# Performance work log

Measured on AMD Instinct MI355X. Metric: run time of the kernel, lower is better.

The kernel has to match this reference:

```python
import jax, jax.numpy as jnp
import numpy as np

L, H, N = 8192, 1024, 1024
MAX_PHASE = 6.283


def setup_inputs() -> dict:
    key = jax.random.key(0)
    ks = jax.random.split(key, 9)
    input_real = jax.random.uniform(ks[0], (L, H), dtype=jnp.float32)
    input_imag = jax.random.uniform(ks[1], (L, H), dtype=jnp.float32)
    # LRU parameter init (r_min=0, r_max=1, max_phase=6.283)
    u1 = jax.random.uniform(ks[2], (N,), dtype=jnp.float32)
    u2 = jax.random.uniform(ks[3], (N,), dtype=jnp.float32)
    nu_log = jnp.log(-0.5 * jnp.log(u1))
    theta_log = jnp.log(u2 * MAX_PHASE)
    B_real = jax.random.normal(ks[4], (N, H), dtype=jnp.float32) / np.float32(np.sqrt(2 * H))
    B_imag = jax.random.normal(ks[5], (N, H), dtype=jnp.float32) / np.float32(np.sqrt(2 * H))
    C_real = jax.random.normal(ks[6], (H, N), dtype=jnp.float32) / np.float32(np.sqrt(N))
    C_imag = jax.random.normal(ks[7], (H, N), dtype=jnp.float32) / np.float32(np.sqrt(N))
    D = jax.random.normal(ks[8], (H,), dtype=jnp.float32)
    diag_lambda = jnp.exp(jax.lax.complex(-jnp.exp(nu_log), jnp.exp(theta_log)))
    gamma_log = jnp.log(jnp.sqrt(1.0 - jnp.abs(diag_lambda) ** 2))
    return dict(input_real=input_real, input_imag=input_imag,
                nu_log=nu_log, theta_log=theta_log,
                B_real=B_real, B_imag=B_imag,
                C_real=C_real, C_imag=C_imag,
                D=D, gamma_log=gamma_log)


def _binop(e_i, e_j):
    a_i, bu_i = e_i
    a_j, bu_j = e_j
    return a_j * a_i, a_j * bu_i + bu_j


def _lru_forward(input_real, input_imag, nu_log, theta_log,
                 B_real, B_imag, C_real, C_imag, D, gamma_log):
    u = jax.lax.complex(input_real, input_imag)                      # (L, H) complex
    Lambda = jnp.exp(jax.lax.complex(-jnp.exp(nu_log), jnp.exp(theta_log)))  # (N,)
    # Faithful to source: exp(i * gamma_log), NOT exp(gamma_log)
    exp_gamma = jnp.exp(jax.lax.complex(jnp.zeros_like(gamma_log), gamma_log))  # (N,)
    B_norm = jax.lax.complex(B_real, B_imag) * exp_gamma[:, None]    # (N, H)
    Bu = jnp.einsum('lh,nh->ln', u, B_norm)                          # (L, N)
    Lambda_el = jnp.broadcast_to(Lambda[None, :], Bu.shape)          # (L, N)
    _, x = jax.lax.associative_scan(_binop, (Lambda_el, Bu))         # (L, N) states
    C = jax.lax.complex(C_real, C_imag)                              # (H, N)
    Dc = D.astype(C.dtype)                                           # (H,) complex
    y = jnp.real(jnp.einsum('ln,hn->lh', x, C)) + jnp.real(Dc[None, :] * u)
    return y                                                         # (L, H) float32


def reference(input_real, input_imag, nu_log, theta_log,
              B_real, B_imag, C_real, C_imag, D, gamma_log):
    return _lru_forward(input_real, input_imag, nu_log, theta_log,
                        B_real, B_imag, C_real, C_imag, D, gamma_log)
```

## Files before the change

kernel.cpp:

```cpp
#include <hip/hip_runtime.h>
#include <math.h>

#define L_SEQ 8192
#define H_DIM 1024
#define N_DIM 1024
#define K2    2048
#define NCHUNK 64
#define CHUNK 128

typedef unsigned short u16;
typedef __attribute__((ext_vector_type(8))) __bf16 bf16x8;
typedef __attribute__((ext_vector_type(4))) float  f32x4;

__device__ __forceinline__ u16 f2bf(float x) {
    unsigned int u = __float_as_uint(x);
    u = (u + 0x7fffu + ((u >> 16) & 1u)) >> 16;
    return (u16)u;
}
__device__ __forceinline__ float bf2f(u16 h) {
    return __uint_as_float(((unsigned int)h) << 16);
}

__device__ __forceinline__ void gload_lds16(const void* g, void* s) {
    __builtin_amdgcn_global_load_lds(
        (const __attribute__((address_space(1))) unsigned int*)g,
        (__attribute__((address_space(3))) unsigned int*)s, 16, 0, 0);
}

__global__ void lru_lambda(const float* __restrict__ nu_log,
                           const float* __restrict__ theta_log,
                           float* __restrict__ Lr, float* __restrict__ Li) {
    int n = blockIdx.x * 256 + threadIdx.x;
    float nu  = expf(nu_log[n]);
    float th  = expf(theta_log[n]);
    float mag = expf(-nu);
    Lr[n] = mag * cosf(th);
    Li[n] = mag * sinf(th);
}

__global__ void pack_u(const float* __restrict__ R, const float* __restrict__ I,
                       u16* __restrict__ A) {
    size_t t = (size_t)blockIdx.x * 256 + threadIdx.x;
    size_t base = t * 4;
    int lrow = (int)(base >> 10);
    int h    = (int)(base & 1023);
    float4 r  = *reinterpret_cast<const float4*>(R + base);
    float4 im = *reinterpret_cast<const float4*>(I + base);
    u16* p0 = A + ((size_t)lrow << 11) + h;
    *reinterpret_cast<ushort4*>(p0) =
        make_ushort4(f2bf(r.x), f2bf(r.y), f2bf(r.z), f2bf(r.w));
    *reinterpret_cast<ushort4*>(p0 + 1024) =
        make_ushort4(f2bf(im.x), f2bf(im.y), f2bf(im.z), f2bf(im.w));
}

__global__ void bnorm_pack(const float* __restrict__ Br, const float* __restrict__ Bi,
                           const float* __restrict__ G, u16* __restrict__ Bp) {
    size_t t = (size_t)blockIdx.x * 256 + threadIdx.x;
    size_t base = t * 4;
    int n = (int)(base >> 10);
    int h = (int)(base & 1023);
    float g = G[n];
    float sg, cg;
    sincosf(g, &sg, &cg);
    float4 br = *reinterpret_cast<const float4*>(Br + base);
    float4 bi = *reinterpret_cast<const float4*>(Bi + base);
    float nr0 = br.x * cg - bi.x * sg, ni0 = br.x * sg + bi.x * cg;
    float nr1 = br.y * cg - bi.y * sg, ni1 = br.y * sg + bi.y * cg;
    float nr2 = br.z * cg - bi.z * sg, ni2 = br.z * sg + bi.z * cg;
    float nr3 = br.w * cg - bi.w * sg, ni3 = br.w * sg + bi.w * cg;
    u16* row0 = Bp + (size_t)n * K2;
    u16* row1 = Bp + (size_t)(N_DIM + n) * K2;
    *reinterpret_cast<ushort4*>(row0 + h) =
        make_ushort4(f2bf(nr0), f2bf(nr1), f2bf(nr2), f2bf(nr3));
    *reinterpret_cast<ushort4*>(row0 + 1024 + h) =
        make_ushort4(f2bf(-ni0), f2bf(-ni1), f2bf(-ni2), f2bf(-ni3));
    *reinterpret_cast<ushort4*>(row1 + h) =
        make_ushort4(f2bf(ni0), f2bf(ni1), f2bf(ni2), f2bf(ni3));
    *reinterpret_cast<ushort4*>(row1 + 1024 + h) =
        make_ushort4(f2bf(nr0), f2bf(nr1), f2bf(nr2), f2bf(nr3));
}

__global__ void pack_C(const float* __restrict__ Cr, const float* __restrict__ Ci,
                       u16* __restrict__ Cp) {
    size_t t = (size_t)blockIdx.x * 256 + threadIdx.x;
    size_t base = t * 4;
    int h = (int)(base >> 10);
    int n = (int)(base & 1023);
    float4 cr = *reinterpret_cast<const float4*>(Cr + base);
    float4 ci = *reinterpret_cast<const float4*>(Ci + base);
    u16* row = Cp + (size_t)h * K2;
    *reinterpret_cast<ushort4*>(row + n) =
        make_ushort4(f2bf(cr.x), f2bf(cr.y), f2bf(cr.z), f2bf(cr.w));
    *reinterpret_cast<ushort4*>(row + 1024 + n) =
        make_ushort4(f2bf(-ci.x), f2bf(-ci.y), f2bf(-ci.z), f2bf(-ci.w));
}

template <int EPI, int WMF>
__global__ __launch_bounds__(512, 2) void gemm_pipe(
    const u16* __restrict__ A, const u16* __restrict__ B, int Klen, int lda,
    u16* __restrict__ OutB, float* __restrict__ OutF, int ldo,
    const float* __restrict__ Dv, const float* __restrict__ Ur) {
    constexpr int BM     = WMF * 32;
    constexpr int BN     = 256;
    constexpr int ABYTES = BM * 128;
    constexpr int SLOT   = (BM + BN) * 128;
    __shared__ __attribute__((aligned(128))) char lds[2 * SLOT];
    const int tid = threadIdx.x;
    const int l   = tid & 63;
    const int w   = tid >> 6;
    const int wm  = w >> 2;
    const int wn  = w & 3;
    const long bm = (long)blockIdx.x * BM;
    const long bn = (long)blockIdx.y * BN;

    f32x4 acc[WMF][4];
#pragma unroll
    for (int i = 0; i < WMF; ++i)
#pragma unroll
        for (int j = 0; j < 4; ++j) acc[i][j] = (f32x4){0.f, 0.f, 0.f, 0.f};

    const int    swzcol    = (((tid & 7) ^ ((tid >> 3) & 7)) << 4);
    const size_t rowstride = (size_t)lda * 2;
    const size_t a_src0    = (size_t)(bm + (tid >> 3)) * rowstride + swzcol;
    const size_t b_src0    = (size_t)(bn + (tid >> 3)) * rowstride + swzcol;
    const char*  Agb       = (const char*)A;
    const char*  Bgb       = (const char*)B;

    auto STAGE = [&](int kt, int sl) {
        const size_t kofs = (size_t)kt * 128;
        char* la = lds + sl * SLOT + tid * 16;
        char* lb = lds + sl * SLOT + ABYTES + tid * 16;
#pragma unroll
        for (int j = 0; j < BM / 64; ++j)
            gload_lds16(Agb + a_src0 + (size_t)j * 64 * rowstride + kofs,
                        la + j * 8192);
#pragma unroll
        for (int j = 0; j < 4; ++j)
            gload_lds16(Bgb + b_src0 + (size_t)j * 64 * rowstride + kofs,
                        lb + j * 8192);
    };

    const int l15   = l & 15;
    const int lslot = l >> 4;

    const int nt = Klen / 64;
    STAGE(0, 0);
    STAGE(1, 1);

    for (int t = 0; t < nt; ++t) {
        const int s = t & 1;
        if (t < nt - 1) {
            if constexpr (BM == 256) asm volatile("s_waitcnt vmcnt(8)" ::: "memory");
            else                     asm volatile("s_waitcnt vmcnt(6)" ::: "memory");
        } else {
            asm volatile("s_waitcnt vmcnt(0)" ::: "memory");
        }
        __builtin_amdgcn_sched_barrier(0);
        __builtin_amdgcn_s_barrier();
        __builtin_amdgcn_sched_barrier(0);

        const char* lA = lds + s * SLOT;
        const char* lB = lA + ABYTES;
#pragma unroll
        for (int kk = 0; kk < 2; ++kk) {
            bf16x8 af[WMF], bg[4];
#pragma unroll
            for (int mi = 0; mi < WMF; ++mi) {
                int r   = wm * (WMF * 16) + mi * 16 + l15;
                int sl3 = ((kk << 2) | lslot) ^ (r & 7);
                af[mi]  = *reinterpret_cast<const bf16x8*>(lA + r * 128 + sl3 * 16);
            }
#pragma unroll
            for (int ni = 0; ni < 4; ++ni) {
                int r   = wn * 64 + ni * 16 + l15;
                int sl3 = ((kk << 2) | lslot) ^ (r & 7);
                bg[ni]  = *reinterpret_cast<const bf16x8*>(lB + r * 128 + sl3 * 16);
            }
            __builtin_amdgcn_s_setprio(1);
#pragma unroll
            for (int mi = 0; mi < WMF; ++mi)
#pragma unroll
                for (int ni = 0; ni < 4; ++ni)
                    acc[mi][ni] = __builtin_amdgcn_mfma_f32_16x16x32_bf16(
                        af[mi], bg[ni], acc[mi][ni], 0, 0, 0);
            __builtin_amdgcn_s_setprio(0);
        }
        __builtin_amdgcn_sched_barrier(0);
        __builtin_amdgcn_s_barrier();
        __builtin_amdgcn_sched_barrier(0);
        if (t + 2 < nt) STAGE(t + 2, s);
    }

#pragma unroll
    for (int mi = 0; mi < WMF; ++mi) {
        const long row0 = bm + wm * (WMF * 16) + mi * 16 + ((l >> 4) << 2);
#pragma unroll
        for (int ni = 0; ni < 4; ++ni) {
            const long col = bn + wn * 64 + ni * 16 + l15;
            if (EPI == 0) {
#pragma unroll
                for (int r = 0; r < 4; ++r)
                    OutB[(size_t)(row0 + r) * ldo + col] = f2bf(acc[mi][ni][r]);
            } else {
                const float d = Dv[col];
#pragma unroll
                for (int r = 0; r < 4; ++r) {
                    size_t o = (size_t)(row0 + r) * ldo + col;
                    OutF[o] = acc[mi][ni][r] + d * Ur[o];
                }
            }
        }
    }
}

__global__ void scan_local(u16* __restrict__ X,
                           const float* __restrict__ Lr, const float* __restrict__ Li,
                           float* __restrict__ Acr, float* __restrict__ Aci,
                           float* __restrict__ bcr, float* __restrict__ bci) {
    int n = blockIdx.y * 256 + threadIdx.x;
    int c = blockIdx.x;
    float lr = Lr[n], li = Li[n];
    float sr = 0.f, si = 0.f, pr = 1.f, pi = 0.f;
    size_t base = (size_t)c * CHUNK * K2 + n;
    for (int j = 0; j < CHUNK; ++j) {
        size_t idx = base + (size_t)j * K2;
        float br = bf2f(X[idx]), bi = bf2f(X[idx + 1024]);
        float nr = lr * sr - li * si + br;
        float ni = lr * si + li * sr + bi;
        sr = nr; si = ni;
        X[idx] = f2bf(sr); X[idx + 1024] = f2bf(si);
        float qr = lr * pr - li * pi;
        float qi = lr * pi + li * pr;
        pr = qr; pi = qi;
    }
    Acr[c * N_DIM + n] = pr; Aci[c * N_DIM + n] = pi;
    bcr[c * N_DIM + n] = sr; bci[c * N_DIM + n] = si;
}

__global__ void scan_carry(const float* __restrict__ Acr, const float* __restrict__ Aci,
                           const float* __restrict__ bcr, const float* __restrict__ bci,
                           float* __restrict__ car, float* __restrict__ cai) {
    int n = blockIdx.x * 256 + threadIdx.x;
    float sr = 0.f, si = 0.f;
    for (int c = 0; c < NCHUNK; ++c) {
        car[c * N_DIM + n] = sr; cai[c * N_DIM + n] = si;
        float ar = Acr[c * N_DIM + n], ai = Aci[c * N_DIM + n];
        float nr = ar * sr - ai * si + bcr[c * N_DIM + n];
        float ni = ar * si + ai * sr + bci[c * N_DIM + n];
        sr = nr; si = ni;
    }
}

__global__ void scan_fix(u16* __restrict__ X,
                         const float* __restrict__ Lr, const float* __restrict__ Li,
                         const float* __restrict__ car, const float* __restrict__ cai) {
    int n = blockIdx.y * 256 + threadIdx.x;
    int c = blockIdx.x + 1;
    float lr = Lr[n], li = Li[n];
    float cr = car[c * N_DIM + n], ci = cai[c * N_DIM + n];
    float pr = lr * cr - li * ci;
    float pi = lr * ci + li * cr;
    size_t base = (size_t)c * CHUNK * K2 + n;
    for (int j = 0; j < CHUNK; ++j) {
        size_t idx = base + (size_t)j * K2;
        X[idx]        = f2bf(bf2f(X[idx]) + pr);
        X[idx + 1024] = f2bf(bf2f(X[idx + 1024]) + pi);
        float qr = lr * pr - li * pi;
        float qi = lr * pi + li * pr;
        pr = qr; pi = qi;
    }
}

extern "C" void kernel_launch(void* const* d_in, const int* in_sizes, int n_in,
                              void* d_out, int out_size, void* d_ws, size_t ws_size,
                              hipStream_t stream) {
    (void)in_sizes; (void)n_in; (void)out_size; (void)ws_size;
    const float* input_real = (const float*)d_in[0];
    const float* input_imag = (const float*)d_in[1];
    const float* nu_log     = (const float*)d_in[2];
    const float* theta_log  = (const float*)d_in[3];
    const float* B_real     = (const float*)d_in[4];
    const float* B_imag     = (const float*)d_in[5];
    const float* C_real     = (const float*)d_in[6];
    const float* C_imag     = (const float*)d_in[7];
    const float* D          = (const float*)d_in[8];
    const float* gamma_log  = (const float*)d_in[9];
    float* y = (float*)d_out;

    char* ws = (char*)d_ws;
    float* Lr  = (float*)(ws);
    float* Li  = (float*)(ws + (4 << 10));
    float* Acr = (float*)(ws + (8 << 10));
    float* Aci = Acr + NCHUNK * N_DIM;
    float* bcr = Aci + NCHUNK * N_DIM;
    float* bci = bcr + NCHUNK * N_DIM;
    float* car = bci + NCHUNK * N_DIM;
    float* cai = car + NCHUNK * N_DIM;
    u16* Ap   = (u16*)(ws + ((size_t)2 << 20));
    u16* Cp   = Ap;
    u16* Bp   = (u16*)(ws + ((size_t)34 << 20));
    u16* X    = (u16*)(ws + ((size_t)42 << 20));

    lru_lambda<<<N_DIM / 256, 256, 0, stream>>>(nu_log, theta_log, Lr, Li);
    pack_u<<<(L_SEQ * H_DIM / 4) / 256, 256, 0, stream>>>(input_real, input_imag, Ap);
    bnorm_pack<<<(N_DIM * H_DIM / 4) / 256, 256, 0, stream>>>(B_real, B_imag, gamma_log, Bp);
    gemm_pipe<0, 8><<<dim3(L_SEQ / 256, K2 / 256), 512, 0, stream>>>(
        Ap, Bp, K2, K2, X, nullptr, K2, nullptr, nullptr);
    scan_local<<<dim3(NCHUNK, N_DIM / 256), 256, 0, stream>>>(X, Lr, Li, Acr, Aci, bcr, bci);
    scan_carry<<<N_DIM / 256, 256, 0, stream>>>(Acr, Aci, bcr, bci, car, cai);
    scan_fix<<<dim3(NCHUNK - 1, N_DIM / 256), 256, 0, stream>>>(X, Lr, Li, car, cai);
    pack_C<<<(H_DIM * N_DIM / 4) / 256, 256, 0, stream>>>(C_real, C_imag, Cp);
    gemm_pipe<1, 4><<<dim3(L_SEQ / 128, H_DIM / 256), 512, 0, stream>>>(
        X, Cp, K2, K2, nullptr, y, H_DIM, D, input_real);
}
```

Baseline: 183.6 us.

## Software-pipeline LDS fragment loads with MFMA in GEMM main loop

Restructures the K-loop so the LDS reads for the next half-tile (kk=1, then the next stage's kk=0) are issued before the MFMAs of the current half-tile. The intent is to hide LDS read latency behind matrix instructions, at the cost of double-buffered fragment registers. The global-to-LDS prefetch waits and barriers are reordered to match. The extra registers can lower occupancy, and the reordered waits and barriers risk subtle races.

```diff
diff --git a/kernel.cpp b/kernel.cpp
--- a/kernel.cpp
+++ b/kernel.cpp
@@ -143,52 +143,76 @@
     const int l15   = l & 15;
     const int lslot = l >> 4;
 
+    auto LOADA = [&](bf16x8 (&af)[WMF], const char* lA, int kk) {
+#pragma unroll
+        for (int mi = 0; mi < WMF; ++mi) {
+            int r   = wm * (WMF * 16) + mi * 16 + l15;
+            int sl3 = ((kk << 2) | lslot) ^ (r & 7);
+            af[mi]  = *reinterpret_cast<const bf16x8*>(lA + r * 128 + sl3 * 16);
+        }
+    };
+    auto LOADB = [&](bf16x8 (&bg)[4], const char* lB, int kk) {
+#pragma unroll
+        for (int ni = 0; ni < 4; ++ni) {
+            int r   = wn * 64 + ni * 16 + l15;
+            int sl3 = ((kk << 2) | lslot) ^ (r & 7);
+            bg[ni]  = *reinterpret_cast<const bf16x8*>(lB + r * 128 + sl3 * 16);
+        }
+    };
+    auto MM = [&](bf16x8 (&af)[WMF], bf16x8 (&bg)[4], int nlo) {
+        __builtin_amdgcn_s_setprio(1);
+#pragma unroll
+        for (int mi = 0; mi < WMF; ++mi)
+#pragma unroll
+            for (int nj = 0; nj < 2; ++nj)
+                acc[mi][nlo + nj] = __builtin_amdgcn_mfma_f32_16x16x32_bf16(
+                    af[mi], bg[nlo + nj], acc[mi][nlo + nj], 0, 0, 0);
+        __builtin_amdgcn_s_setprio(0);
+    };
+
     const int nt = Klen / 64;
     STAGE(0, 0);
     STAGE(1, 1);
+    if constexpr (BM == 256) asm volatile("s_waitcnt vmcnt(8)" ::: "memory");
+    else                     asm volatile("s_waitcnt vmcnt(6)" ::: "memory");
+    __builtin_amdgcn_sched_barrier(0);
+    __builtin_amdgcn_s_barrier();
+    __builtin_amdgcn_sched_barrier(0);
+
+    bf16x8 afX[WMF], afY[WMF], bgX[4], bgY[4];
+    LOADA(afX, lds, 0);
+    LOADB(bgX, lds + ABYTES, 0);
 
     for (int t = 0; t < nt; ++t) {
         const int s = t & 1;
-        if (t < nt - 1) {
-            if constexpr (BM == 256) asm volatile("s_waitcnt vmcnt(8)" ::: "memory");
-            else                     asm volatile("s_waitcnt vmcnt(6)" ::: "memory");
-        } else {
-            asm volatile("s_waitcnt vmcnt(0)" ::: "memory");
-        }
+        const char* lA = lds + s * SLOT;
+        const char* lB = lA + ABYTES;
+        LOADA(afY, lA, 1);
+        LOADB(bgY, lB, 1);
+        MM(afX, bgX, 0);
+        MM(afX, bgX, 2);
+        asm volatile("s_waitcnt lgkmcnt(0)" ::: "memory");
         __builtin_amdgcn_sched_barrier(0);
         __builtin_amdgcn_s_barrier();
         __builtin_amdgcn_sched_barrier(0);
-
-        const char* lA = lds + s * SLOT;
-        const char* lB = lA + ABYTES;
-#pragma unroll
-        for (int kk = 0; kk < 2; ++kk) {
-            bf16x8 af[WMF], bg[4];
-#pragma unroll
-            for (int mi = 0; mi < WMF; ++mi) {
-                int r   = wm * (WMF * 16) + mi * 16 + l15;
-                int sl3 = ((kk << 2) | lslot) ^ (r & 7);
-                af[mi]  = *reinterpret_cast<const bf16x8*>(lA + r * 128 + sl3 * 16);
-            }
-#pragma unroll
-            for (int ni = 0; ni < 4; ++ni) {
-                int r   = wn * 64 + ni * 16 + l15;
-                int sl3 = ((kk << 2) | lslot) ^ (r & 7);
-                bg[ni]  = *reinterpret_cast<const bf16x8*>(lB + r * 128 + sl3 * 16);
-            }
-            __builtin_amdgcn_s_setprio(1);
-#pragma unroll
-            for (int mi = 0; mi < WMF; ++mi)
-#pragma unroll
-                for (int ni = 0; ni < 4; ++ni)
-                    acc[mi][ni] = __builtin_amdgcn_mfma_f32_16x16x32_bf16(
-                        af[mi], bg[ni], acc[mi][ni], 0, 0, 0);
-            __builtin_amdgcn_s_setprio(0);
-        }
-        __builtin_amdgcn_sched_barrier(0);
-        __builtin_amdgcn_s_barrier();
-        __builtin_amdgcn_sched_barrier(0);
-        if (t + 2 < nt) STAGE(t + 2, s);
+        if (t + 2 < nt) {
+            STAGE(t + 2, s);
+            if constexpr (BM == 256) asm volatile("s_waitcnt vmcnt(8)" ::: "memory");
+            else                     asm volatile("s_waitcnt vmcnt(6)" ::: "memory");
+        } else if (t + 1 < nt) {
+            asm volatile("s_waitcnt vmcnt(0)" ::: "memory");
+        }
+        if (t + 1 < nt) {
+            __builtin_amdgcn_sched_barrier(0);
+            __builtin_amdgcn_s_barrier();
+            __builtin_amdgcn_sched_barrier(0);
+            const char* lA2 = lds + (s ^ 1) * SLOT;
+            const char* lB2 = lA2 + ABYTES;
+            LOADA(afX, lA2, 0);
+            LOADB(bgX, lB2, 0);
+        }
+        MM(afY, bgY, 0);
+        MM(afY, bgY, 2);
     }
 
 #pragma unroll
```

Result: no change. 182.4 us (-0.6%).

## Restructure GEMM main loop into 8-phase quadrant pipeline with split staging

Applied to the files above, without the earlier changes.

Replaces the simple double-buffered K loop in both GEMMs with an 8-phase schedule. Each phase loads a half-tile of A or B into LDS, reads register fragments for the next quadrant, and issues MFMAs on one quadrant of the output tile. The aim is to interleave global-to-LDS loads, LDS reads and MFMA work more finely so memory latency hides behind compute. In exchange it adds a barrier and an lgkmcnt wait per phase, and it uses more registers for the ping-pong fragment sets.

```diff
diff --git a/kernel.cpp b/kernel.cpp
--- a/kernel.cpp
+++ b/kernel.cpp
@@ -96,22 +96,24 @@
 }
 
 template <int EPI, int WMF>
-__global__ __launch_bounds__(512, 2) void gemm_pipe(
+__global__ __launch_bounds__(512, 2) void gemm8p(
     const u16* __restrict__ A, const u16* __restrict__ B, int Klen, int lda,
     u16* __restrict__ OutB, float* __restrict__ OutF, int ldo,
     const float* __restrict__ Dv, const float* __restrict__ Ur) {
-    constexpr int BM     = WMF * 32;
-    constexpr int BN     = 256;
-    constexpr int ABYTES = BM * 128;
-    constexpr int SLOT   = (BM + BN) * 128;
-    __shared__ __attribute__((aligned(128))) char lds[2 * SLOT];
+    constexpr int BM    = WMF * 32;
+    constexpr int AMF   = WMF / 2;
+    constexpr int GA    = BM / 128;
+    constexpr int AH    = (BM / 2) * 128;
+    constexpr int BH    = 16384;
+    constexpr int DBUFB = 2 * AH + 2 * BH;
+    __shared__ __attribute__((aligned(128))) char lds[2 * DBUFB];
     const int tid = threadIdx.x;
     const int l   = tid & 63;
     const int w   = tid >> 6;
     const int wm  = w >> 2;
     const int wn  = w & 3;
     const long bm = (long)blockIdx.x * BM;
-    const long bn = (long)blockIdx.y * BN;
+    const long bn = (long)blockIdx.y * 256;
 
     f32x4 acc[WMF][4];
 #pragma unroll
@@ -119,77 +121,154 @@
 #pragma unroll
         for (int j = 0; j < 4; ++j) acc[i][j] = (f32x4){0.f, 0.f, 0.f, 0.f};
 
-    const int    swzcol    = (((tid & 7) ^ ((tid >> 3) & 7)) << 4);
+    const int lr  = tid >> 3;
+    const int lrh = lr >> 5, lrl = lr & 31;
+    const int swzcol = ((tid & 7) ^ (lr & 7)) << 4;
     const size_t rowstride = (size_t)lda * 2;
-    const size_t a_src0    = (size_t)(bm + (tid >> 3)) * rowstride + swzcol;
-    const size_t b_src0    = (size_t)(bn + (tid >> 3)) * rowstride + swzcol;
-    const char*  Agb       = (const char*)A;
-    const char*  Bgb       = (const char*)B;
-
-    auto STAGE = [&](int kt, int sl) {
-        const size_t kofs = (size_t)kt * 128;
-        char* la = lds + sl * SLOT + tid * 16;
-        char* lb = lds + sl * SLOT + ABYTES + tid * 16;
-#pragma unroll
-        for (int j = 0; j < BM / 64; ++j)
-            gload_lds16(Agb + a_src0 + (size_t)j * 64 * rowstride + kofs,
-                        la + j * 8192);
-#pragma unroll
-        for (int j = 0; j < 4; ++j)
-            gload_lds16(Bgb + b_src0 + (size_t)j * 64 * rowstride + kofs,
-                        lb + j * 8192);
-    };
+    const char* Agb = (const char*)A;
+    const char* Bgb = (const char*)B;
+    size_t a_src[2][GA];
+#pragma unroll
+    for (int h = 0; h < 2; ++h)
+#pragma unroll
+        for (int j = 0; j < GA; ++j) {
+            int row = (BM == 256) ? (j * 128 + h * 64 + lr)
+                                  : (lrh * 64 + h * 32 + lrl);
+            a_src[h][j] = (size_t)(bm + row) * rowstride + swzcol;
+        }
+    size_t b_src[2][2];
+#pragma unroll
+    for (int h = 0; h < 2; ++h)
+#pragma unroll
+        for (int j = 0; j < 2; ++j) {
+            int row = j * 128 + lrh * 64 + h * 32 + lrl;
+            b_src[h][j] = (size_t)(bn + row) * rowstride + swzcol;
+        }
 
     const int l15   = l & 15;
     const int lslot = l >> 4;
-
-    const int nt = Klen / 64;
-    STAGE(0, 0);
-    STAGE(1, 1);
-
-    for (int t = 0; t < nt; ++t) {
-        const int s = t & 1;
-        if (t < nt - 1) {
-            if constexpr (BM == 256) asm volatile("s_waitcnt vmcnt(8)" ::: "memory");
-            else                     asm volatile("s_waitcnt vmcnt(6)" ::: "memory");
-        } else {
-            asm volatile("s_waitcnt vmcnt(0)" ::: "memory");
-        }
-        __builtin_amdgcn_sched_barrier(0);
-        __builtin_amdgcn_s_barrier();
-        __builtin_amdgcn_sched_barrier(0);
-
-        const char* lA = lds + s * SLOT;
-        const char* lB = lA + ABYTES;
+    int aoff[AMF][2], boff[2][2];
+#pragma unroll
+    for (int mi = 0; mi < AMF; ++mi)
 #pragma unroll
         for (int kk = 0; kk < 2; ++kk) {
-            bf16x8 af[WMF], bg[4];
-#pragma unroll
-            for (int mi = 0; mi < WMF; ++mi) {
-                int r   = wm * (WMF * 16) + mi * 16 + l15;
-                int sl3 = ((kk << 2) | lslot) ^ (r & 7);
-                af[mi]  = *reinterpret_cast<const bf16x8*>(lA + r * 128 + sl3 * 16);
-            }
-#pragma unroll
-            for (int ni = 0; ni < 4; ++ni) {
-                int r   = wn * 64 + ni * 16 + l15;
-                int sl3 = ((kk << 2) | lslot) ^ (r & 7);
-                bg[ni]  = *reinterpret_cast<const bf16x8*>(lB + r * 128 + sl3 * 16);
-            }
-            __builtin_amdgcn_s_setprio(1);
-#pragma unroll
-            for (int mi = 0; mi < WMF; ++mi)
-#pragma unroll
-                for (int ni = 0; ni < 4; ++ni)
-                    acc[mi][ni] = __builtin_amdgcn_mfma_f32_16x16x32_bf16(
-                        af[mi], bg[ni], acc[mi][ni], 0, 0, 0);
-            __builtin_amdgcn_s_setprio(0);
-        }
-        __builtin_amdgcn_sched_barrier(0);
-        __builtin_amdgcn_s_barrier();
-        __builtin_amdgcn_sched_barrier(0);
-        if (t + 2 < nt) STAGE(t + 2, s);
-    }
+            int rr = wm * (BM / 4) + mi * 16 + l15;
+            aoff[mi][kk] = rr * 128 + ((((kk << 2) | lslot) ^ (rr & 7)) << 4);
+        }
+#pragma unroll
+    for (int ni = 0; ni < 2; ++ni)
+#pragma unroll
+        for (int kk = 0; kk < 2; ++kk) {
+            int rr = wn * 32 + ni * 16 + l15;
+            boff[ni][kk] = rr * 128 + ((((kk << 2) | lslot) ^ (rr & 7)) << 4);
+        }
+
+    const int nt    = Klen / 64;
+    const int niter = nt / 2;
+
+    bf16x8 aE[2 * AMF], aO[2 * AMF], bE[4], bO[4];
+
+#define STAGE_A(KT, H) do { if ((KT) < nt) {                                 \
+    char* _d = lds + ((KT) & 1) * DBUFB + (H) * AH + tid * 16;               \
+    _Pragma("unroll") for (int j = 0; j < GA; ++j)                           \
+        gload_lds16(Agb + a_src[H][j] + (size_t)(KT) * 128, _d + j * 8192);  \
+    } } while (0)
+#define STAGE_B(KT, H) do { if ((KT) < nt) {                                 \
+    char* _d = lds + ((KT) & 1) * DBUFB + 2 * AH + (H) * BH + tid * 16;      \
+    _Pragma("unroll") for (int j = 0; j < 2; ++j)                            \
+        gload_lds16(Bgb + b_src[H][j] + (size_t)(KT) * 128, _d + j * 8192);  \
+    } } while (0)
+#define READ_A(DST, QM, DB) {                                                \
+    _Pragma("unroll") for (int mi = 0; mi < AMF; ++mi)                       \
+        _Pragma("unroll") for (int kk = 0; kk < 2; ++kk)                     \
+            DST[mi * 2 + kk] = *reinterpret_cast<const bf16x8*>(             \
+                lds + (DB) * DBUFB + (QM) * AH + aoff[mi][kk]); }
+#define READ_B(DST, QN, DB) {                                                \
+    _Pragma("unroll") for (int ni = 0; ni < 2; ++ni)                         \
+        _Pragma("unroll") for (int kk = 0; kk < 2; ++kk)                     \
+            DST[ni * 2 + kk] = *reinterpret_cast<const bf16x8*>(             \
+                lds + (DB) * DBUFB + 2 * AH + (QN) * BH + boff[ni][kk]); }
+#define MFMA_Q(ASET, BSET, QM, QN) {                                         \
+    __builtin_amdgcn_s_setprio(1);                                           \
+    _Pragma("unroll") for (int mi = 0; mi < AMF; ++mi)                       \
+        _Pragma("unroll") for (int ni = 0; ni < 2; ++ni)                     \
+            _Pragma("unroll") for (int kk = 0; kk < 2; ++kk)                 \
+                acc[(QM) * AMF + mi][(QN) * 2 + ni] =                        \
+                    __builtin_amdgcn_mfma_f32_16x16x32_bf16(                 \
+                        ASET[mi * 2 + kk], BSET[ni * 2 + kk],                \
+                        acc[(QM) * AMF + mi][(QN) * 2 + ni], 0, 0, 0);       \
+    __builtin_amdgcn_s_setprio(0); }
+#define VMW do { if constexpr (WMF == 8)                                     \
+        asm volatile("s_waitcnt vmcnt(6)" ::: "memory");                     \
+    else asm volatile("s_waitcnt vmcnt(4)" ::: "memory"); } while (0)
+#define BAR1 do { __builtin_amdgcn_sched_barrier(0);                         \
+    __builtin_amdgcn_s_barrier();                                            \
+    __builtin_amdgcn_sched_barrier(0); } while (0)
+#define ENDPH do { asm volatile("s_waitcnt lgkmcnt(0)" ::: "memory");        \
+    __builtin_amdgcn_sched_barrier(0);                                       \
+    __builtin_amdgcn_s_barrier();                                            \
+    __builtin_amdgcn_sched_barrier(0); } while (0)
+
+    STAGE_B(0, 0); STAGE_A(0, 0); STAGE_A(0, 1); STAGE_B(0, 1);
+    STAGE_B(1, 0); STAGE_A(1, 0); STAGE_A(1, 1);
+    VMW;
+    BAR1;
+    READ_A(aE, 0, 0); READ_B(bE, 0, 0);
+    asm volatile("s_waitcnt lgkmcnt(0)" ::: "memory");
+
+    for (int i = 0; i < niter; ++i) {
+        const int t2 = 2 * i;
+        STAGE_B(t2 + 1, 1);
+        BAR1;
+        READ_A(aO, 1, 0);
+        MFMA_Q(aE, bE, 0, 0);
+        ENDPH;
+        STAGE_B(t2 + 2, 0);
+        BAR1;
+        READ_B(bO, 1, 0);
+        MFMA_Q(aO, bE, 1, 0);
+        ENDPH;
+        STAGE_A(t2 + 2, 0);
+        BAR1;
+        MFMA_Q(aE, bO, 0, 1);
+        ENDPH;
+        STAGE_A(t2 + 2, 1);
+        if (i + 1 < niter) { VMW; }
+        else { asm volatile("s_waitcnt vmcnt(0)" ::: "memory"); }
+        BAR1;
+        READ_A(aE, 0, 1); READ_B(bE, 0, 1);
+        MFMA_Q(aO, bO, 1, 1);
+        ENDPH;
+        STAGE_B(t2 + 2, 1);
+        BAR1;
+        READ_A(aO, 1, 1);
+        MFMA_Q(aE, bE, 0, 0);
+        ENDPH;
+        STAGE_B(t2 + 3, 0);
+        BAR1;
+        READ_B(bO, 1, 1);
+        MFMA_Q(aO, bE, 1, 0);
+        ENDPH;
+        STAGE_A(t2 + 3, 0);
+        BAR1;
+        MFMA_Q(aE, bO, 0, 1);
+        ENDPH;
+        STAGE_A(t2 + 3, 1);
+        VMW;
+        BAR1;
+        if (i + 1 < niter) { READ_A(aE, 0, 0); READ_B(bE, 0, 0); }
+        MFMA_Q(aO, bO, 1, 1);
+        ENDPH;
+    }
+
+#undef STAGE_A
+#undef STAGE_B
+#undef READ_A
+#undef READ_B
+#undef MFMA_Q
+#undef VMW
+#undef BAR1
+#undef ENDPH
 
 #pragma unroll
     for (int mi = 0; mi < WMF; ++mi) {
@@ -304,12 +383,12 @@
     lru_lambda<<<N_DIM / 256, 256, 0, stream>>>(nu_log, theta_log, Lr, Li);
     pack_u<<<(L_SEQ * H_DIM / 4) / 256, 256, 0, stream>>>(input_real, input_imag, Ap);
     bnorm_pack<<<(N_DIM * H_DIM / 4) / 256, 256, 0, stream>>>(B_real, B_imag, gamma_log, Bp);
-    gemm_pipe<0, 8><<<dim3(L_SEQ / 256, K2 / 256), 512, 0, stream>>>(
+    gemm8p<0, 8><<<dim3(L_SEQ / 256, K2 / 256), 512, 0, stream>>>(
         Ap, Bp, K2, K2, X, nullptr, K2, nullptr, nullptr);
     scan_local<<<dim3(NCHUNK, N_DIM / 256), 256, 0, stream>>>(X, Lr, Li, Acr, Aci, bcr, bci);
     scan_carry<<<N_DIM / 256, 256, 0, stream>>>(Acr, Aci, bcr, bci, car, cai);
     scan_fix<<<dim3(NCHUNK - 1, N_DIM / 256), 256, 0, stream>>>(X, Lr, Li, car, cai);
     pack_C<<<(H_DIM * N_DIM / 4) / 256, 256, 0, stream>>>(C_real, C_imag, Cp);
-    gemm_pipe<1, 4><<<dim3(L_SEQ / 128, H_DIM / 256), 512, 0, stream>>>(
+    gemm8p<1, 4><<<dim3(L_SEQ / 128, H_DIM / 256), 512, 0, stream>>>(
         X, Cp, K2, K2, nullptr, y, H_DIM, D, input_real);
 }
```

Result: slower. 187.5 us (+2.1%).

## Restructure chunked scan to reduce-then-apply and retile output GEMM

Applied to the files above, without the earlier changes.

The chunked scan becomes a two-pass reduce/apply scheme. The first pass now only reads X to build chunk summaries and no longer writes it back. The apply pass recomputes the full recurrence from each carry, which cuts one full read-write sweep of the bf16 state buffer. Lambda is computed inline in each scan kernel, removing the separate lambda kernel. The second GEMM moves to a 128x128 tile with 256 threads, giving more blocks for better CU occupancy at the cost of less data reuse per block.

```diff
diff --git a/kernel.cpp b/kernel.cpp
--- a/kernel.cpp
+++ b/kernel.cpp
@@ -25,17 +25,6 @@
     __builtin_amdgcn_global_load_lds(
         (const __attribute__((address_space(1))) unsigned int*)g,
         (__attribute__((address_space(3))) unsigned int*)s, 16, 0, 0);
-}
-
-__global__ void lru_lambda(const float* __restrict__ nu_log,
-                           const float* __restrict__ theta_log,
-                           float* __restrict__ Lr, float* __restrict__ Li) {
-    int n = blockIdx.x * 256 + threadIdx.x;
-    float nu  = expf(nu_log[n]);
-    float th  = expf(theta_log[n]);
-    float mag = expf(-nu);
-    Lr[n] = mag * cosf(th);
-    Li[n] = mag * sinf(th);
 }
 
 __global__ void pack_u(const float* __restrict__ R, const float* __restrict__ I,
@@ -95,15 +84,12 @@
         make_ushort4(f2bf(-ci.x), f2bf(-ci.y), f2bf(-ci.z), f2bf(-ci.w));
 }
 
-template <int EPI, int WMF>
 __global__ __launch_bounds__(512, 2) void gemm_pipe(
     const u16* __restrict__ A, const u16* __restrict__ B, int Klen, int lda,
-    u16* __restrict__ OutB, float* __restrict__ OutF, int ldo,
-    const float* __restrict__ Dv, const float* __restrict__ Ur) {
-    constexpr int BM     = WMF * 32;
-    constexpr int BN     = 256;
+    u16* __restrict__ OutB, int ldo) {
+    constexpr int BM     = 256;
     constexpr int ABYTES = BM * 128;
-    constexpr int SLOT   = (BM + BN) * 128;
+    constexpr int SLOT   = (BM + 256) * 128;
     __shared__ __attribute__((aligned(128))) char lds[2 * SLOT];
     const int tid = threadIdx.x;
     const int l   = tid & 63;
@@ -111,11 +97,11 @@
     const int wm  = w >> 2;
     const int wn  = w & 3;
     const long bm = (long)blockIdx.x * BM;
-    const long bn = (long)blockIdx.y * BN;
-
-    f32x4 acc[WMF][4];
-#pragma unroll
-    for (int i = 0; i < WMF; ++i)
+    const long bn = (long)blockIdx.y * 256;
+
+    f32x4 acc[8][4];
+#pragma unroll
+    for (int i = 0; i < 8; ++i)
 #pragma unroll
         for (int j = 0; j < 4; ++j) acc[i][j] = (f32x4){0.f, 0.f, 0.f, 0.f};
 
@@ -131,7 +117,7 @@
         char* la = lds + sl * SLOT + tid * 16;
         char* lb = lds + sl * SLOT + ABYTES + tid * 16;
 #pragma unroll
-        for (int j = 0; j < BM / 64; ++j)
+        for (int j = 0; j < 4; ++j)
             gload_lds16(Agb + a_src0 + (size_t)j * 64 * rowstride + kofs,
                         la + j * 8192);
 #pragma unroll
@@ -149,12 +135,8 @@
 
     for (int t = 0; t < nt; ++t) {
         const int s = t & 1;
-        if (t < nt - 1) {
-            if constexpr (BM == 256) asm volatile("s_waitcnt vmcnt(8)" ::: "memory");
-            else                     asm volatile("s_waitcnt vmcnt(6)" ::: "memory");
-        } else {
-            asm volatile("s_waitcnt vmcnt(0)" ::: "memory");
-        }
+        if (t < nt - 1) asm volatile("s_waitcnt vmcnt(8)" ::: "memory");
+        else            asm volatile("s_waitcnt vmcnt(0)" ::: "memory");
         __builtin_amdgcn_sched_barrier(0);
         __builtin_amdgcn_s_barrier();
         __builtin_amdgcn_sched_barrier(0);
@@ -163,10 +145,10 @@
         const char* lB = lA + ABYTES;
 #pragma unroll
         for (int kk = 0; kk < 2; ++kk) {
-            bf16x8 af[WMF], bg[4];
-#pragma unroll
-            for (int mi = 0; mi < WMF; ++mi) {
-                int r   = wm * (WMF * 16) + mi * 16 + l15;
+            bf16x8 af[8], bg[4];
+#pragma unroll
+            for (int mi = 0; mi < 8; ++mi) {
+                int r   = wm * 128 + mi * 16 + l15;
                 int sl3 = ((kk << 2) | lslot) ^ (r & 7);
                 af[mi]  = *reinterpret_cast<const bf16x8*>(lA + r * 128 + sl3 * 16);
             }
@@ -178,7 +160,7 @@
             }
             __builtin_amdgcn_s_setprio(1);
 #pragma unroll
-            for (int mi = 0; mi < WMF; ++mi)
+            for (int mi = 0; mi < 8; ++mi)
 #pragma unroll
                 for (int ni = 0; ni < 4; ++ni)
                     acc[mi][ni] = __builtin_amdgcn_mfma_f32_16x16x32_bf16(
@@ -192,34 +174,136 @@
     }
 
 #pragma unroll
-    for (int mi = 0; mi < WMF; ++mi) {
-        const long row0 = bm + wm * (WMF * 16) + mi * 16 + ((l >> 4) << 2);
+    for (int mi = 0; mi < 8; ++mi) {
+        const long row0 = bm + wm * 128 + mi * 16 + ((l >> 4) << 2);
 #pragma unroll
         for (int ni = 0; ni < 4; ++ni) {
             const long col = bn + wn * 64 + ni * 16 + l15;
-            if (EPI == 0) {
-#pragma unroll
-                for (int r = 0; r < 4; ++r)
-                    OutB[(size_t)(row0 + r) * ldo + col] = f2bf(acc[mi][ni][r]);
-            } else {
-                const float d = Dv[col];
-#pragma unroll
-                for (int r = 0; r < 4; ++r) {
-                    size_t o = (size_t)(row0 + r) * ldo + col;
-                    OutF[o] = acc[mi][ni][r] + d * Ur[o];
-                }
+#pragma unroll
+            for (int r = 0; r < 4; ++r)
+                OutB[(size_t)(row0 + r) * ldo + col] = f2bf(acc[mi][ni][r]);
+        }
+    }
+}
+
+__global__ __launch_bounds__(256, 2) void gemm_small(
+    const u16* __restrict__ A, const u16* __restrict__ B, int Klen, int lda,
+    float* __restrict__ OutF, int ldo,
+    const float* __restrict__ Dv, const float* __restrict__ Ur) {
+    constexpr int ABYTES = 128 * 128;
+    constexpr int SLOT   = 2 * ABYTES;
+    __shared__ __attribute__((aligned(128))) char lds[2 * SLOT];
+    const int tid = threadIdx.x;
+    const int l   = tid & 63;
+    const int w   = tid >> 6;
+    const int wm  = w >> 1;
+    const int wn  = w & 1;
+    const long bm = (long)blockIdx.x * 128;
+    const long bn = (long)blockIdx.y * 128;
+
+    f32x4 acc[4][4];
+#pragma unroll
+    for (int i = 0; i < 4; ++i)
+#pragma unroll
+        for (int j = 0; j < 4; ++j) acc[i][j] = (f32x4){0.f, 0.f, 0.f, 0.f};
+
+    const int    lr        = tid >> 3;
+    const int    swzcol    = (((tid & 7) ^ (lr & 7)) << 4);
+    const size_t rowstride = (size_t)lda * 2;
+    const size_t a_src0    = (size_t)(bm + lr) * rowstride + swzcol;
+    const size_t b_src0    = (size_t)(bn + lr) * rowstride + swzcol;
+    const char*  Agb       = (const char*)A;
+    const char*  Bgb       = (const char*)B;
+
+    auto STAGE = [&](int kt, int sl) {
+        const size_t kofs = (size_t)kt * 128;
+        char* la = lds + sl * SLOT + tid * 16;
+        char* lb = lds + sl * SLOT + ABYTES + tid * 16;
+#pragma unroll
+        for (int j = 0; j < 4; ++j)
+            gload_lds16(Agb + a_src0 + (size_t)j * 32 * rowstride + kofs,
+                        la + j * 4096);
+#pragma unroll
+        for (int j = 0; j < 4; ++j)
+            gload_lds16(Bgb + b_src0 + (size_t)j * 32 * rowstride + kofs,
+                        lb + j * 4096);
+    };
+
+    const int l15   = l & 15;
+    const int lslot = l >> 4;
+
+    const int nt = Klen / 64;
+    STAGE(0, 0);
+    STAGE(1, 1);
+
+    for (int t = 0; t < nt; ++t) {
+        const int s = t & 1;
+        if (t < nt - 1) asm volatile("s_waitcnt vmcnt(8)" ::: "memory");
+        else            asm volatile("s_waitcnt vmcnt(0)" ::: "memory");
+        __builtin_amdgcn_sched_barrier(0);
+        __builtin_amdgcn_s_barrier();
+        __builtin_amdgcn_sched_barrier(0);
+
+        const char* lA = lds + s * SLOT;
+        const char* lB = lA + ABYTES;
+#pragma unroll
+        for (int kk = 0; kk < 2; ++kk) {
+            bf16x8 af[4], bg[4];
+#pragma unroll
+            for (int mi = 0; mi < 4; ++mi) {
+                int r   = wm * 64 + mi * 16 + l15;
+                int sl3 = ((kk << 2) | lslot) ^ (r & 7);
+                af[mi]  = *reinterpret_cast<const bf16x8*>(lA + r * 128 + sl3 * 16);
+            }
+#pragma unroll
+            for (int ni = 0; ni < 4; ++ni) {
+                int r   = wn * 64 + ni * 16 + l15;
+                int sl3 = ((kk << 2) | lslot) ^ (r & 7);
+                bg[ni]  = *reinterpret_cast<const bf16x8*>(lB + r * 128 + sl3 * 16);
+            }
+            __builtin_amdgcn_s_setprio(1);
+#pragma unroll
+            for (int mi = 0; mi < 4; ++mi)
+#pragma unroll
+                for (int ni = 0; ni < 4; ++ni)
+                    acc[mi][ni] = __builtin_amdgcn_mfma_f32_16x16x32_bf16(
+                        af[mi], bg[ni], acc[mi][ni], 0, 0, 0);
+            __builtin_amdgcn_s_setprio(0);
+        }
+        __builtin_amdgcn_sched_barrier(0);
+        __builtin_amdgcn_s_barrier();
+        __builtin_amdgcn_sched_barrier(0);
+        if (t + 2 < nt) STAGE(t + 2, s);
+    }
+
+#pragma unroll
+    for (int mi = 0; mi < 4; ++mi) {
+        const long row0 = bm + wm * 64 + mi * 16 + ((l >> 4) << 2);
+#pragma unroll
+        for (int ni = 0; ni < 4; ++ni) {
+            const long col = bn + wn * 64 + ni * 16 + l15;
+            const float d = Dv[col];
+#pragma unroll
+            for (int r = 0; r < 4; ++r) {
+                size_t o = (size_t)(row0 + r) * ldo + col;
+                OutF[o] = acc[mi][ni][r] + d * Ur[o];
             }
         }
     }
 }
 
-__global__ void scan_local(u16* __restrict__ X,
-                           const float* __restrict__ Lr, const float* __restrict__ Li,
-                           float* __restrict__ Acr, float* __restrict__ Aci,
-                           float* __restrict__ bcr, float* __restrict__ bci) {
+__global__ void scan_sum(const u16* __restrict__ X,
+                         const float* __restrict__ nu_log,
+                         const float* __restrict__ theta_log,
+                         float* __restrict__ Acr, float* __restrict__ Aci,
+                         float* __restrict__ bcr, float* __restrict__ bci) {
     int n = blockIdx.y * 256 + threadIdx.x;
     int c = blockIdx.x;
-    float lr = Lr[n], li = Li[n];
+    float mag = expf(-expf(nu_log[n]));
+    float th  = expf(theta_log[n]);
+    float sg, cg;
+    sincosf(th, &sg, &cg);
+    float lr = mag * cg, li = mag * sg;
     float sr = 0.f, si = 0.f, pr = 1.f, pi = 0.f;
     size_t base = (size_t)c * CHUNK * K2 + n;
     for (int j = 0; j < CHUNK; ++j) {
@@ -228,7 +312,6 @@
         float nr = lr * sr - li * si + br;
         float ni = lr * si + li * sr + bi;
         sr = nr; si = ni;
-        X[idx] = f2bf(sr); X[idx + 1024] = f2bf(si);
         float qr = lr * pr - li * pi;
         float qi = lr * pi + li * pr;
         pr = qr; pi = qi;
@@ -251,23 +334,26 @@
     }
 }
 
-__global__ void scan_fix(u16* __restrict__ X,
-                         const float* __restrict__ Lr, const float* __restrict__ Li,
-                         const float* __restrict__ car, const float* __restrict__ cai) {
+__global__ void scan_apply(u16* __restrict__ X,
+                           const float* __restrict__ nu_log,
+                           const float* __restrict__ theta_log,
+                           const float* __restrict__ car, const float* __restrict__ cai) {
     int n = blockIdx.y * 256 + threadIdx.x;
-    int c = blockIdx.x + 1;
-    float lr = Lr[n], li = Li[n];
-    float cr = car[c * N_DIM + n], ci = cai[c * N_DIM + n];
-    float pr = lr * cr - li * ci;
-    float pi = lr * ci + li * cr;
+    int c = blockIdx.x;
+    float mag = expf(-expf(nu_log[n]));
+    float th  = expf(theta_log[n]);
+    float sg, cg;
+    sincosf(th, &sg, &cg);
+    float lr = mag * cg, li = mag * sg;
+    float sr = car[c * N_DIM + n], si = cai[c * N_DIM + n];
     size_t base = (size_t)c * CHUNK * K2 + n;
     for (int j = 0; j < CHUNK; ++j) {
         size_t idx = base + (size_t)j * K2;
-        X[idx]        = f2bf(bf2f(X[idx]) + pr);
-        X[idx + 1024] = f2bf(bf2f(X[idx + 1024]) + pi);
-        float qr = lr * pr - li * pi;
-        float qi = lr * pi + li * pr;
-        pr = qr; pi = qi;
+        float br = bf2f(X[idx]), bi = bf2f(X[idx + 1024]);
+        float nr = lr * sr - li * si + br;
+        float ni = lr * si + li * sr + bi;
+        sr = nr; si = ni;
+        X[idx] = f2bf(sr); X[idx + 1024] = f2bf(si);
     }
 }
 
@@ -288,8 +374,6 @@
     float* y = (float*)d_out;
 
     char* ws = (char*)d_ws;
-    float* Lr  = (float*)(ws);
-    float* Li  = (float*)(ws + (4 << 10));
     float* Acr = (float*)(ws + (8 << 10));
     float* Aci = Acr + NCHUNK * N_DIM;
     float* bcr = Aci + NCHUNK * N_DIM;
@@ -301,15 +385,16 @@
     u16* Bp   = (u16*)(ws + ((size_t)34 << 20));
     u16* X    = (u16*)(ws + ((size_t)42 << 20));
 
-    lru_lambda<<<N_DIM / 256, 256, 0, stream>>>(nu_log, theta_log, Lr, Li);
     pack_u<<<(L_SEQ * H_DIM / 4) / 256, 256, 0, stream>>>(input_real, input_imag, Ap);
     bnorm_pack<<<(N_DIM * H_DIM / 4) / 256, 256, 0, stream>>>(B_real, B_imag, gamma_log, Bp);
-    gemm_pipe<0, 8><<<dim3(L_SEQ / 256, K2 / 256), 512, 0, stream>>>(
-        Ap, Bp, K2, K2, X, nullptr, K2, nullptr, nullptr);
-    scan_local<<<dim3(NCHUNK, N_DIM / 256), 256, 0, stream>>>(X, Lr, Li, Acr, Aci, bcr, bci);
+    gemm_pipe<<<dim3(L_SEQ / 256, K2 / 256), 512, 0, stream>>>(
+        Ap, Bp, K2, K2, X, K2);
+    scan_sum<<<dim3(NCHUNK, N_DIM / 256), 256, 0, stream>>>(
+        X, nu_log, theta_log, Acr, Aci, bcr, bci);
     scan_carry<<<N_DIM / 256, 256, 0, stream>>>(Acr, Aci, bcr, bci, car, cai);
-    scan_fix<<<dim3(NCHUNK - 1, N_DIM / 256), 256, 0, stream>>>(X, Lr, Li, car, cai);
+    scan_apply<<<dim3(NCHUNK, N_DIM / 256), 256, 0, stream>>>(
+        X, nu_log, theta_log, car, cai);
     pack_C<<<(H_DIM * N_DIM / 4) / 256, 256, 0, stream>>>(C_real, C_imag, Cp);
-    gemm_pipe<1, 4><<<dim3(L_SEQ / 128, H_DIM / 256), 512, 0, stream>>>(
-        X, Cp, K2, K2, nullptr, y, H_DIM, D, input_real);
-}
+    gemm_small<<<dim3(L_SEQ / 128, H_DIM / 128), 256, 0, stream>>>(
+        X, Cp, K2, K2, y, H_DIM, D, input_real);
+}
```

Measured after the change: 171.8 us. 6.4% less time.
